# Optimization experiments

Measured on AMD Instinct MI355X. Metric: run time of the kernel, lower is better.

## Reference

```python
import jax, jax.numpy as jnp
import numpy as np

B, C, T = 8, 128, 32768
OUT, K, DIL = 128, 2, 2


def dilated_indices(T, k, d):
    # Faithful vectorized version of the original Python double loop:
    # idx[span*k + j] = span + j*d, clamped to T (the zero-pad slot) when >= T+1.
    padded = T + 1
    idx = jnp.arange(padded)[:, None] + jnp.arange(k)[None, :] * d  # (padded, k)
    idx = idx.reshape(-1)                                           # (k*padded,)
    return jnp.where(idx >= padded, T, idx)


def setup_inputs() -> dict:
    key = jax.random.key(0)
    k1, k2, k3 = jax.random.split(key, 3)
    x = jax.random.normal(k1, (B, C, T), dtype=jnp.float32)
    # Conv1d(in=C, out=OUT, kernel_size=K) parameters
    W = jax.random.normal(k2, (OUT, C, K), dtype=jnp.float32) * 0.05
    b = jax.random.normal(k3, (OUT,), dtype=jnp.float32) * 0.05
    return {"x": x, "W": W, "b": b}


def reference(x, W, b):
    Bx, Cx, Tx = x.shape
    # pad one zero column at the end of the time axis (torch.cat with zeros)
    xp = jnp.concatenate([x, jnp.zeros((Bx, Cx, 1), x.dtype)], axis=2)  # (B,C,T+1)
    idx = dilated_indices(Tx, K, DIL)                                   # (K*(T+1),)
    swizzle = xp[:, :, idx]                                             # (B,C,K*(T+1))
    # Conv1d with stride == kernel_size over the swizzled buffer is a GEMM
    # over non-overlapping windows of size K.
    sw = swizzle.reshape(Bx, Cx, Tx + 1, K)                             # (B,C,T+1,K)
    out = jnp.einsum('bcpk,ock->bop', sw, W) + b[None, :, None]         # (B,OUT,T+1)
    return out
```

## Files before the change

### kernel.cpp

```cpp
#include <hip/hip_runtime.h>


namespace {

constexpr int kB   = 8;
constexpr int kC   = 128;
constexpr int kT   = 32768;
constexpr int kP   = kT + 1;
constexpr int kOut = 128;
constexpr int kNP  = 64;
constexpr int kNTiles = (kP + kNP - 1) / kNP;
constexpr int kLStride = 136;

typedef __attribute__((ext_vector_type(8))) short short8;
typedef __attribute__((ext_vector_type(4))) float f32x4;

__device__ inline short f2bf(float f) {
    unsigned int u = __builtin_bit_cast(unsigned int, f);
    u += 0x7fffu + ((u >> 16) & 1u);
    return (short)(u >> 16);
}

__global__ __launch_bounds__(256, 2) void dconv_mfma(
    const float* __restrict__ x, const float* __restrict__ W,
    const float* __restrict__ bias, float* __restrict__ out)
{
    __shared__ __align__(16) short xs[66 * kLStride];

    const int tid  = threadIdx.x;
    const int lane = tid & 63;
    const int wv   = tid >> 6;
    const int bb   = blockIdx.x / kNTiles;
    const int tile = blockIdx.x % kNTiles;
    const int p0   = tile * kNP;

    {
        const float* xb = x + (size_t)bb * kC * kT;
        const int cg = tid >> 6;
        const int nrep = ((tid & 63) < 2) ? 2 : 1;
        for (int rep = 0; rep < nrep; ++rep) {
            const int pos = (tid & 63) + rep * 64;
            const int gp  = p0 + pos;
            const bool ok = gp < kT;
            const float* col = xb + gp;
            #pragma unroll
            for (int i = 0; i < 4; ++i) {
                const int c0 = cg * 32 + i * 8;
                short8 v;
                #pragma unroll
                for (int j = 0; j < 8; ++j) {
                    const float f = ok ? col[(size_t)(c0 + j) * kT] : 0.0f;
                    v[j] = f2bf(f);
                }
                *reinterpret_cast<short8*>(xs + pos * kLStride + c0) = v;
            }
        }
    }

    const int rowbase = wv * 32;
    short8 wf[2][2][4];
    #pragma unroll
    for (int cc = 0; cc < 2; ++cc) {
        const int o = rowbase + cc * 16 + (lane & 15);
        #pragma unroll
        for (int s = 0; s < 4; ++s) {
            const int cb = s * 32 + (lane >> 4) * 8;
            const float4* wp = reinterpret_cast<const float4*>(W + o * (kC * 2) + cb * 2);
            short8 f0, f1;
            #pragma unroll
            for (int q = 0; q < 4; ++q) {
                const float4 v = wp[q];
                f0[q * 2 + 0] = f2bf(v.x);  f1[q * 2 + 0] = f2bf(v.y);
                f0[q * 2 + 1] = f2bf(v.z);  f1[q * 2 + 1] = f2bf(v.w);
            }
            wf[0][cc][s] = f0;
            wf[1][cc][s] = f1;
        }
    }

    f32x4 acc[2][4];
    #pragma unroll
    for (int cc = 0; cc < 2; ++cc) {
        const int ob = rowbase + cc * 16 + (lane >> 4) * 4;
        f32x4 a;
        a[0] = bias[ob + 0]; a[1] = bias[ob + 1];
        a[2] = bias[ob + 2]; a[3] = bias[ob + 3];
        #pragma unroll
        for (int nc = 0; nc < 4; ++nc) acc[cc][nc] = a;
    }

    __syncthreads();

    #pragma unroll
    for (int tap = 0; tap < 2; ++tap) {
        #pragma unroll
        for (int s = 0; s < 4; ++s) {
            const int cb = s * 32 + (lane >> 4) * 8;
            #pragma unroll
            for (int nc = 0; nc < 4; ++nc) {
                const int pos = nc * 16 + (lane & 15) + 2 * tap;
                const short8 bf = *reinterpret_cast<const short8*>(xs + pos * kLStride + cb);
                acc[0][nc] = __builtin_amdgcn_mfma_f32_16x16x32_bf16(wf[tap][0][s], bf, acc[0][nc], 0, 0, 0);
                acc[1][nc] = __builtin_amdgcn_mfma_f32_16x16x32_bf16(wf[tap][1][s], bf, acc[1][nc], 0, 0, 0);
            }
        }
    }

    float* ob = out + (size_t)bb * kOut * kP;
    #pragma unroll
    for (int nc = 0; nc < 4; ++nc) {
        const int col = p0 + nc * 16 + (lane & 15);
        if (col < kP) {
            #pragma unroll
            for (int cc = 0; cc < 2; ++cc) {
                const int orow = rowbase + cc * 16 + (lane >> 4) * 4;
                #pragma unroll
                for (int r = 0; r < 4; ++r) {
                    ob[(size_t)(orow + r) * kP + col] = acc[cc][nc][r];
                }
            }
        }
    }
}

}

extern "C" void kernel_launch(void* const* d_in, const int* in_sizes, int n_in,
                              void* d_out, int out_size, void* d_ws, size_t ws_size,
                              hipStream_t stream) {
    const float* x    = (const float*)d_in[0];
    const float* W    = (const float*)d_in[1];
    const float* bias = (const float*)d_in[2];
    float* out        = (float*)d_out;

    dim3 grid(kB * kNTiles);
    dim3 block(256);
    hipLaunchKernelGGL(dconv_mfma, grid, block, 0, stream, x, W, bias, out);
}
```

Measured before the change: 349.9 us.

## Double time-tile width and restructure staging with unguarded fast path

Raises the positions per block from 64 to 128, which halves the block count and reduces the halo overhead and the per-block reload and convert of weights. Staging is rewritten so each thread loads eight channels into registers before converting, with a template that drops bounds checks for interior tiles. Weight loads are hoisted ahead of the conversion, and the x staging now follows the weight fetch. The accumulators double to 16 f32x4 per thread, which raises register pressure under launch_bounds(256,2).

```diff
diff --git a/kernel.cpp b/kernel.cpp
--- a/kernel.cpp
+++ b/kernel.cpp
@@ -8,24 +8,62 @@
 constexpr int kT   = 32768;
 constexpr int kP   = kT + 1;
 constexpr int kOut = 128;
-constexpr int kNP  = 64;
+constexpr int kNP  = 128;
 constexpr int kNTiles = (kP + kNP - 1) / kNP;
 constexpr int kLStride = 136;
 
 typedef __attribute__((ext_vector_type(8))) short short8;
 typedef __attribute__((ext_vector_type(4))) float f32x4;
 
-__device__ inline short f2bf(float f) {
+__device__ __forceinline__ short f2bf(float f) {
     unsigned int u = __builtin_bit_cast(unsigned int, f);
     u += 0x7fffu + ((u >> 16) & 1u);
     return (short)(u >> 16);
+}
+
+template <bool GUARD>
+__device__ __forceinline__ void stage_tile(const float* __restrict__ xb,
+                                           short* __restrict__ xs,
+                                           int tid, int p0) {
+    {
+        const int pos = tid & 127;
+        const int gp  = p0 + pos;
+        const bool ok = !GUARD || (gp < kT);
+        const float* col = xb + (ok ? gp : 0);
+        const int c0base = (tid >> 7) * 64;
+        #pragma unroll
+        for (int ch = 0; ch < 8; ++ch) {
+            const int c0 = c0base + ch * 8;
+            float r[8];
+            #pragma unroll
+            for (int j = 0; j < 8; ++j) r[j] = col[(c0 + j) << 15];
+            short8 v;
+            #pragma unroll
+            for (int j = 0; j < 8; ++j) v[j] = ok ? f2bf(r[j]) : (short)0;
+            *reinterpret_cast<short8*>(xs + pos * kLStride + c0) = v;
+        }
+    }
+    if (tid < 32) {
+        const int pos = 128 + (tid & 1);
+        const int gp  = p0 + pos;
+        const bool ok = !GUARD || (gp < kT);
+        const float* col = xb + (ok ? gp : 0);
+        const int c0 = (tid >> 1) * 8;
+        float r[8];
+        #pragma unroll
+        for (int j = 0; j < 8; ++j) r[j] = col[(c0 + j) << 15];
+        short8 v;
+        #pragma unroll
+        for (int j = 0; j < 8; ++j) v[j] = ok ? f2bf(r[j]) : (short)0;
+        *reinterpret_cast<short8*>(xs + pos * kLStride + c0) = v;
+    }
 }
 
 __global__ __launch_bounds__(256, 2) void dconv_mfma(
     const float* __restrict__ x, const float* __restrict__ W,
     const float* __restrict__ bias, float* __restrict__ out)
 {
-    __shared__ __align__(16) short xs[66 * kLStride];
+    __shared__ __align__(16) short xs[130 * kLStride];
 
     const int tid  = threadIdx.x;
     const int lane = tid & 63;
@@ -33,29 +71,6 @@
     const int bb   = blockIdx.x / kNTiles;
     const int tile = blockIdx.x % kNTiles;
     const int p0   = tile * kNP;
-
-    {
-        const float* xb = x + (size_t)bb * kC * kT;
-        const int cg = tid >> 6;
-        const int nrep = ((tid & 63) < 2) ? 2 : 1;
-        for (int rep = 0; rep < nrep; ++rep) {
-            const int pos = (tid & 63) + rep * 64;
-            const int gp  = p0 + pos;
-            const bool ok = gp < kT;
-            const float* col = xb + gp;
-            #pragma unroll
-            for (int i = 0; i < 4; ++i) {
-                const int c0 = cg * 32 + i * 8;
-                short8 v;
-                #pragma unroll
-                for (int j = 0; j < 8; ++j) {
-                    const float f = ok ? col[(size_t)(c0 + j) * kT] : 0.0f;
-                    v[j] = f2bf(f);
-                }
-                *reinterpret_cast<short8*>(xs + pos * kLStride + c0) = v;
-            }
-        }
-    }
 
     const int rowbase = wv * 32;
     short8 wf[2][2][4];
@@ -66,19 +81,25 @@
         for (int s = 0; s < 4; ++s) {
             const int cb = s * 32 + (lane >> 4) * 8;
             const float4* wp = reinterpret_cast<const float4*>(W + o * (kC * 2) + cb * 2);
+            float4 wr[4];
+            #pragma unroll
+            for (int q = 0; q < 4; ++q) wr[q] = wp[q];
             short8 f0, f1;
             #pragma unroll
             for (int q = 0; q < 4; ++q) {
-                const float4 v = wp[q];
-                f0[q * 2 + 0] = f2bf(v.x);  f1[q * 2 + 0] = f2bf(v.y);
-                f0[q * 2 + 1] = f2bf(v.z);  f1[q * 2 + 1] = f2bf(v.w);
+                f0[q * 2 + 0] = f2bf(wr[q].x);  f1[q * 2 + 0] = f2bf(wr[q].y);
+                f0[q * 2 + 1] = f2bf(wr[q].z);  f1[q * 2 + 1] = f2bf(wr[q].w);
             }
             wf[0][cc][s] = f0;
             wf[1][cc][s] = f1;
         }
     }
 
-    f32x4 acc[2][4];
+    const float* xb = x + (size_t)bb * kC * kT;
+    if (p0 + 129 < kT) stage_tile<false>(xb, xs, tid, p0);
+    else               stage_tile<true>(xb, xs, tid, p0);
+
+    f32x4 acc[2][8];
     #pragma unroll
     for (int cc = 0; cc < 2; ++cc) {
         const int ob = rowbase + cc * 16 + (lane >> 4) * 4;
@@ -86,7 +107,7 @@
         a[0] = bias[ob + 0]; a[1] = bias[ob + 1];
         a[2] = bias[ob + 2]; a[3] = bias[ob + 3];
         #pragma unroll
-        for (int nc = 0; nc < 4; ++nc) acc[cc][nc] = a;
+        for (int nc = 0; nc < 8; ++nc) acc[cc][nc] = a;
     }
 
     __syncthreads();
@@ -97,7 +118,7 @@
         for (int s = 0; s < 4; ++s) {
             const int cb = s * 32 + (lane >> 4) * 8;
             #pragma unroll
-            for (int nc = 0; nc < 4; ++nc) {
+            for (int nc = 0; nc < 8; ++nc) {
                 const int pos = nc * 16 + (lane & 15) + 2 * tap;
                 const short8 bf = *reinterpret_cast<const short8*>(xs + pos * kLStride + cb);
                 acc[0][nc] = __builtin_amdgcn_mfma_f32_16x16x32_bf16(wf[tap][0][s], bf, acc[0][nc], 0, 0, 0);
@@ -108,7 +129,7 @@
 
     float* ob = out + (size_t)bb * kOut * kP;
     #pragma unroll
-    for (int nc = 0; nc < 4; ++nc) {
+    for (int nc = 0; nc < 8; ++nc) {
         const int col = p0 + nc * 16 + (lane & 15);
         if (col < kP) {
             #pragma unroll
```

Measured after the change: 281.6 us. 1.24x faster.
